# Performance work log

Hardware: AMD Instinct MI355X
Metric: run time of the kernel (lower is better)

Reference implementation:

```python
import jax, jax.numpy as jnp
import numpy as np

HEADS = 8
BUCKET_SIZE = 128
KV_BUCKET_SIZE = 128
DIM = 64
TEMPERATURE = 0.7
SINKHORN_ITER = 8
EPS = 1e-6


def _log(t):
    # matches torch `log(t, eps=1e-6) = torch.log(t + eps)`
    return jnp.log(t + EPS)


def setup_inputs() -> dict:
    key = jax.random.key(0)
    k1, k2, k3 = jax.random.split(key, 3)
    q = jax.random.normal(k1, (32, 8192, 64), dtype=jnp.float32)
    k = jax.random.normal(k2, (32, 8192, 64), dtype=jnp.float32)
    # uniform sample used to build gumbel noise (deterministic substitute for
    # torch's in-module uniform_ sampling); shape == R shape [bh, buckets, kv_buckets]
    u_gumbel = jax.random.uniform(k3, (32, 64, 64), dtype=jnp.float32)
    return {"q": q, "k": k, "u_gumbel": u_gumbel, "topk": 1}


def reference(q, k, u_gumbel, topk):
    bh, q_len, dim = q.shape
    buckets = q_len // BUCKET_SIZE          # 64
    kv_buckets = k.shape[1] // KV_BUCKET_SIZE  # 64

    # bucket then mean over bucket contents -> [bh, buckets, dim]
    sq = q.reshape(bh, buckets, BUCKET_SIZE, dim).mean(axis=2)
    sk = k.reshape(bh, kv_buckets, KV_BUCKET_SIZE, dim).mean(axis=2)

    # bucket-to-bucket similarity [bh, buckets, kv_buckets]
    R = jnp.einsum('bie,bje->bij', sq, sk) * (DIM ** -0.5)

    # gumbel_sinkhorn(F.relu(R), sinkhorn_iter, temperature)
    r = _log(jax.nn.relu(R))
    gumbel = -_log(-_log(u_gumbel))
    r = (r + gumbel) / TEMPERATURE

    # sinkhorn normalization: alternate col/row log-space normalization
    for _ in range(SINKHORN_ITER):
        r = r - jax.scipy.special.logsumexp(r, axis=2, keepdims=True)
        r = r - jax.scipy.special.logsumexp(r, axis=1, keepdims=True)
    return jnp.exp(r)
```

## Files before the change

### kernel.cpp

```cpp
#include <hip/hip_runtime.h>
#include <hip/hip_bf16.h>
#include <math.h>

#define EPSF 1e-6f

__global__ __launch_bounds__(256) void bucket_mean_kernel(
    const float* __restrict__ q,
    const float* __restrict__ k,
    float* __restrict__ sqk)
{
    int b      = blockIdx.x;
    int t      = b >> 11;
    int rem    = b & 2047;
    int bh     = rem >> 6;
    int bucket = rem & 63;

    const float* src = t ? k : q;
    const float4* base = reinterpret_cast<const float4*>(
        src + ((size_t)bh * 8192 + (size_t)bucket * 128) * 64);

    int c  = threadIdx.x & 15;
    int rr = threadIdx.x >> 4;

    float4 acc = make_float4(0.f, 0.f, 0.f, 0.f);
    #pragma unroll
    for (int j = rr; j < 128; j += 16) {
        float4 v = base[j * 16 + c];
        acc.x += v.x; acc.y += v.y; acc.z += v.z; acc.w += v.w;
    }

    __shared__ float4 red[256];
    red[threadIdx.x] = acc;
    __syncthreads();

    #pragma unroll
    for (int s = 128; s >= 16; s >>= 1) {
        if (threadIdx.x < (unsigned)s) {
            float4 o = red[threadIdx.x + s];
            float4 m = red[threadIdx.x];
            m.x += o.x; m.y += o.y; m.z += o.z; m.w += o.w;
            red[threadIdx.x] = m;
        }
        __syncthreads();
    }

    if (threadIdx.x < 16) {
        float4 m = red[threadIdx.x];
        const float inv = 1.0f / 128.0f;
        m.x *= inv; m.y *= inv; m.z *= inv; m.w *= inv;
        float4* dst = reinterpret_cast<float4*>(
            sqk + (size_t)t * 32 * 64 * 64 + ((size_t)bh * 64 + bucket) * 64);
        dst[threadIdx.x] = m;
    }
}

__global__ __launch_bounds__(256) void sinkhorn_kernel(
    const float* __restrict__ sqk,
    const float* __restrict__ u_gumbel,
    float* __restrict__ out)
{
    int bh = blockIdx.x;

    __shared__ float sq_s[64][65];
    __shared__ float sk_s[64][65];
    __shared__ float r_s[64][65];

    const float* sqp = sqk + (size_t)bh * 4096;
    const float* skp = sqk + (size_t)32 * 4096 + (size_t)bh * 4096;

    #pragma unroll
    for (int t = 0; t < 16; ++t) {
        int idx = threadIdx.x + 256 * t;
        int i = idx >> 6, e = idx & 63;
        sq_s[i][e] = sqp[idx];
        sk_s[i][e] = skp[idx];
    }
    __syncthreads();

    const float scale = 0.125f;
    const float invT  = 1.0f / 0.7f;
    #pragma unroll 4
    for (int t = 0; t < 16; ++t) {
        int idx = threadIdx.x + 256 * t;
        int i = idx >> 6, j = idx & 63;
        float acc = 0.f;
        #pragma unroll
        for (int e = 0; e < 64; ++e)
            acc = fmaf(sq_s[i][e], sk_s[j][e], acc);
        float R  = acc * scale;
        float rl = fmaxf(R, 0.f);
        float u  = u_gumbel[(size_t)bh * 4096 + idx];
        float g  = -logf(-logf(u + EPSF) + EPSF);
        r_s[i][j] = (logf(rl + EPSF) + g) * invT;
    }
    __syncthreads();

    int lane4 = threadIdx.x & 3;
    int rc    = threadIdx.x >> 2;
    for (int it = 0; it < 8; ++it) {
        {
            float m = -INFINITY;
            #pragma unroll
            for (int t = 0; t < 16; ++t) m = fmaxf(m, r_s[rc][lane4 * 16 + t]);
            m = fmaxf(m, __shfl_xor(m, 1, 64));
            m = fmaxf(m, __shfl_xor(m, 2, 64));
            float s = 0.f;
            #pragma unroll
            for (int t = 0; t < 16; ++t) s += expf(r_s[rc][lane4 * 16 + t] - m);
            s += __shfl_xor(s, 1, 64);
            s += __shfl_xor(s, 2, 64);
            float lse = m + logf(s);
            #pragma unroll
            for (int t = 0; t < 16; ++t) r_s[rc][lane4 * 16 + t] -= lse;
        }
        __syncthreads();
        {
            float m = -INFINITY;
            #pragma unroll
            for (int t = 0; t < 16; ++t) m = fmaxf(m, r_s[lane4 * 16 + t][rc]);
            m = fmaxf(m, __shfl_xor(m, 1, 64));
            m = fmaxf(m, __shfl_xor(m, 2, 64));
            float s = 0.f;
            #pragma unroll
            for (int t = 0; t < 16; ++t) s += expf(r_s[lane4 * 16 + t][rc] - m);
            s += __shfl_xor(s, 1, 64);
            s += __shfl_xor(s, 2, 64);
            float lse = m + logf(s);
            #pragma unroll
            for (int t = 0; t < 16; ++t) r_s[lane4 * 16 + t][rc] -= lse;
        }
        __syncthreads();
    }

    #pragma unroll
    for (int t = 0; t < 16; ++t) {
        int idx = threadIdx.x + 256 * t;
        int i = idx >> 6, j = idx & 63;
        out[(size_t)bh * 4096 + idx] = expf(r_s[i][j]);
    }
}

extern "C" void kernel_launch(void* const* d_in, const int* in_sizes, int n_in,
                              void* d_out, int out_size, void* d_ws, size_t ws_size,
                              hipStream_t stream) {
    const float* q = (const float*)d_in[0];
    const float* k = (const float*)d_in[1];
    const float* u = (const float*)d_in[2];
    float* out = (float*)d_out;
    float* sqk = (float*)d_ws;

    bucket_mean_kernel<<<4096, 256, 0, stream>>>(q, k, sqk);
    sinkhorn_kernel<<<32, 256, 0, stream>>>(sqk, u, out);
}
```

Baseline: 177.1 us.

## Use wave-per-bucket mean reduction and 1024-thread Sinkhorn with fast math

The bucket-mean kernel now gives each 64-lane wave one bucket and reduces with cross-lane shuffles. This removes the shared-memory tree reduction and its barriers, and launches four buckets per block. The Sinkhorn kernel grows to 1024 threads per block: each thread computes four R entries with register blocking, and row/column logsumexp uses 16 lanes of 4 elements each. Fast __expf/__logf intrinsics replace the precise functions. This trades a little numerical accuracy for more parallelism in the 32-block serial stage.

```diff
diff --git a/kernel.cpp b/kernel.cpp
--- a/kernel.cpp
+++ b/kernel.cpp
@@ -9,57 +9,51 @@
     const float* __restrict__ k,
     float* __restrict__ sqk)
 {
-    int b      = blockIdx.x;
-    int t      = b >> 11;
-    int rem    = b & 2047;
-    int bh     = rem >> 6;
-    int bucket = rem & 63;
+    int g      = blockIdx.x * 4 + (threadIdx.x >> 6);
+    int t      = g >> 11;
+    int bh     = (g >> 6) & 31;
+    int bucket = g & 63;
 
     const float* src = t ? k : q;
     const float4* base = reinterpret_cast<const float4*>(
         src + ((size_t)bh * 8192 + (size_t)bucket * 128) * 64);
 
-    int c  = threadIdx.x & 15;
-    int rr = threadIdx.x >> 4;
+    int lane = threadIdx.x & 63;
+    int rr   = lane >> 4;
+    int c    = lane & 15;
 
     float4 acc = make_float4(0.f, 0.f, 0.f, 0.f);
-    #pragma unroll
-    for (int j = rr; j < 128; j += 16) {
-        float4 v = base[j * 16 + c];
+    #pragma unroll 8
+    for (int j = 0; j < 32; ++j) {
+        float4 v = base[(rr + j * 4) * 16 + c];
         acc.x += v.x; acc.y += v.y; acc.z += v.z; acc.w += v.w;
     }
 
-    __shared__ float4 red[256];
-    red[threadIdx.x] = acc;
-    __syncthreads();
+    acc.x += __shfl_xor(acc.x, 16, 64);
+    acc.y += __shfl_xor(acc.y, 16, 64);
+    acc.z += __shfl_xor(acc.z, 16, 64);
+    acc.w += __shfl_xor(acc.w, 16, 64);
+    acc.x += __shfl_xor(acc.x, 32, 64);
+    acc.y += __shfl_xor(acc.y, 32, 64);
+    acc.z += __shfl_xor(acc.z, 32, 64);
+    acc.w += __shfl_xor(acc.w, 32, 64);
 
-    #pragma unroll
-    for (int s = 128; s >= 16; s >>= 1) {
-        if (threadIdx.x < (unsigned)s) {
-            float4 o = red[threadIdx.x + s];
-            float4 m = red[threadIdx.x];
-            m.x += o.x; m.y += o.y; m.z += o.z; m.w += o.w;
-            red[threadIdx.x] = m;
-        }
-        __syncthreads();
-    }
-
-    if (threadIdx.x < 16) {
-        float4 m = red[threadIdx.x];
+    if (lane < 16) {
         const float inv = 1.0f / 128.0f;
-        m.x *= inv; m.y *= inv; m.z *= inv; m.w *= inv;
+        acc.x *= inv; acc.y *= inv; acc.z *= inv; acc.w *= inv;
         float4* dst = reinterpret_cast<float4*>(
             sqk + (size_t)t * 32 * 64 * 64 + ((size_t)bh * 64 + bucket) * 64);
-        dst[threadIdx.x] = m;
+        dst[c] = acc;
     }
 }
 
-__global__ __launch_bounds__(256) void sinkhorn_kernel(
+__global__ __launch_bounds__(1024) void sinkhorn_kernel(
     const float* __restrict__ sqk,
     const float* __restrict__ u_gumbel,
     float* __restrict__ out)
 {
-    int bh = blockIdx.x;
+    int bh  = blockIdx.x;
+    int tid = threadIdx.x;
 
     __shared__ float sq_s[64][65];
     __shared__ float sk_s[64][65];
@@ -69,74 +63,93 @@
     const float* skp = sqk + (size_t)32 * 4096 + (size_t)bh * 4096;
 
     #pragma unroll
-    for (int t = 0; t < 16; ++t) {
-        int idx = threadIdx.x + 256 * t;
+    for (int t = 0; t < 4; ++t) {
+        int idx = tid + 1024 * t;
         int i = idx >> 6, e = idx & 63;
         sq_s[i][e] = sqp[idx];
         sk_s[i][e] = skp[idx];
     }
     __syncthreads();
 
-    const float scale = 0.125f;
-    const float invT  = 1.0f / 0.7f;
-    #pragma unroll 4
-    for (int t = 0; t < 16; ++t) {
-        int idx = threadIdx.x + 256 * t;
-        int i = idx >> 6, j = idx & 63;
-        float acc = 0.f;
+    {
+        int j  = tid & 63;
+        int i0 = tid >> 6;
+        float acc0 = 0.f, acc1 = 0.f, acc2 = 0.f, acc3 = 0.f;
         #pragma unroll
-        for (int e = 0; e < 64; ++e)
-            acc = fmaf(sq_s[i][e], sk_s[j][e], acc);
-        float R  = acc * scale;
-        float rl = fmaxf(R, 0.f);
-        float u  = u_gumbel[(size_t)bh * 4096 + idx];
-        float g  = -logf(-logf(u + EPSF) + EPSF);
-        r_s[i][j] = (logf(rl + EPSF) + g) * invT;
+        for (int e = 0; e < 64; ++e) {
+            float s = sk_s[j][e];
+            acc0 = fmaf(sq_s[i0][e],      s, acc0);
+            acc1 = fmaf(sq_s[i0 + 16][e], s, acc1);
+            acc2 = fmaf(sq_s[i0 + 32][e], s, acc2);
+            acc3 = fmaf(sq_s[i0 + 48][e], s, acc3);
+        }
+        const float scale = 0.125f;
+        const float invT  = 1.0f / 0.7f;
+        float accs[4] = {acc0, acc1, acc2, acc3};
+        #pragma unroll
+        for (int t = 0; t < 4; ++t) {
+            int i   = i0 + 16 * t;
+            float R = accs[t] * scale;
+            float rl = fmaxf(R, 0.f);
+            float u  = u_gumbel[(size_t)bh * 4096 + i * 64 + j];
+            float gm = -__logf(-__logf(u + EPSF) + EPSF);
+            r_s[i][j] = (__logf(rl + EPSF) + gm) * invT;
+        }
     }
     __syncthreads();
 
-    int lane4 = threadIdx.x & 3;
-    int rc    = threadIdx.x >> 2;
+    int lane16 = tid & 15;
+    int rc     = tid >> 4;
+    int cbase  = lane16 * 4;
     for (int it = 0; it < 8; ++it) {
         {
-            float m = -INFINITY;
-            #pragma unroll
-            for (int t = 0; t < 16; ++t) m = fmaxf(m, r_s[rc][lane4 * 16 + t]);
+            float v0 = r_s[rc][cbase + 0], v1 = r_s[rc][cbase + 1];
+            float v2 = r_s[rc][cbase + 2], v3 = r_s[rc][cbase + 3];
+            float m = fmaxf(fmaxf(v0, v1), fmaxf(v2, v3));
             m = fmaxf(m, __shfl_xor(m, 1, 64));
             m = fmaxf(m, __shfl_xor(m, 2, 64));
-            float s = 0.f;
-            #pragma unroll
-            for (int t = 0; t < 16; ++t) s += expf(r_s[rc][lane4 * 16 + t] - m);
+            m = fmaxf(m, __shfl_xor(m, 4, 64));
+            m = fmaxf(m, __shfl_xor(m, 8, 64));
+            float s = __expf(v0 - m) + __expf(v1 - m)
+                    + __expf(v2 - m) + __expf(v3 - m);
             s += __shfl_xor(s, 1, 64);
             s += __shfl_xor(s, 2, 64);
-            float lse = m + logf(s);
-            #pragma unroll
-            for (int t = 0; t < 16; ++t) r_s[rc][lane4 * 16 + t] -= lse;
+            s += __shfl_xor(s, 4, 64);
+            s += __shfl_xor(s, 8, 64);
+            float lse = m + __logf(s);
+            r_s[rc][cbase + 0] = v0 - lse;
+            r_s[rc][cbase + 1] = v1 - lse;
+            r_s[rc][cbase + 2] = v2 - lse;
+            r_s[rc][cbase + 3] = v3 - lse;
         }
         __syncthreads();
         {
-            float m = -INFINITY;
-            #pragma unroll
-            for (int t = 0; t < 16; ++t) m = fmaxf(m, r_s[lane4 * 16 + t][rc]);
+            float v0 = r_s[cbase + 0][rc], v1 = r_s[cbase + 1][rc];
+            float v2 = r_s[cbase + 2][rc], v3 = r_s[cbase + 3][rc];
+            float m = fmaxf(fmaxf(v0, v1), fmaxf(v2, v3));
             m = fmaxf(m, __shfl_xor(m, 1, 64));
             m = fmaxf(m, __shfl_xor(m, 2, 64));
-            float s = 0.f;
-            #pragma unroll
-            for (int t = 0; t < 16; ++t) s += expf(r_s[lane4 * 16 + t][rc] - m);
+            m = fmaxf(m, __shfl_xor(m, 4, 64));
+            m = fmaxf(m, __shfl_xor(m, 8, 64));
+            float s = __expf(v0 - m) + __expf(v1 - m)
+                    + __expf(v2 - m) + __expf(v3 - m);
             s += __shfl_xor(s, 1, 64);
             s += __shfl_xor(s, 2, 64);
-            float lse = m + logf(s);
-            #pragma unroll
-            for (int t = 0; t < 16; ++t) r_s[lane4 * 16 + t][rc] -= lse;
+            s += __shfl_xor(s, 4, 64);
+            s += __shfl_xor(s, 8, 64);
+            float lse = m + __logf(s);
+            r_s[cbase + 0][rc] = v0 - lse;
+            r_s[cbase + 1][rc] = v1 - lse;
+            r_s[cbase + 2][rc] = v2 - lse;
+            r_s[cbase + 3][rc] = v3 - lse;
         }
         __syncthreads();
     }
 
     #pragma unroll
-    for (int t = 0; t < 16; ++t) {
-        int idx = threadIdx.x + 256 * t;
-        int i = idx >> 6, j = idx & 63;
-        out[(size_t)bh * 4096 + idx] = expf(r_s[i][j]);
+    for (int t = 0; t < 4; ++t) {
+        int idx = tid + 1024 * t;
+        out[(size_t)bh * 4096 + idx] = __expf(r_s[idx >> 6][idx & 63]);
     }
 }
 
@@ -149,6 +162,6 @@
     float* out = (float*)d_out;
     float* sqk = (float*)d_ws;
 
-    bucket_mean_kernel<<<4096, 256, 0, stream>>>(q, k, sqk);
-    sinkhorn_kernel<<<32, 256, 0, stream>>>(sqk, u, out);
+    bucket_mean_kernel<<<1024, 256, 0, stream>>>(q, k, sqk);
+    sinkhorn_kernel<<<32, 1024, 0, stream>>>(sqk, u, out);
 }
```

Measured after the change: 166.5 us. 1.06x faster.
